# Kernel optimization log

Hardware: AMD Instinct MI355X
Metric: run time of the kernel (lower is better)

The kernel has to match this reference:

```python
import jax, jax.numpy as jnp
import numpy as np

ALPHA = 0.2  # LeakyReLU negative slope


def setup_inputs() -> dict:
    key = jax.random.key(0)
    k1, k2, k3, k4, k5 = jax.random.split(key, 5)
    N, H, W, T, V, F = 8, 64, 64, 32, 32, 32
    h = jax.random.normal(k1, (N, H, W, T, V), dtype=jnp.float32)
    W_map = jax.random.normal(k2, (T, F), dtype=jnp.float32) * (1.414 / np.sqrt(T))
    b_map = jax.random.normal(k3, (F,), dtype=jnp.float32) * 0.01
    a_attn = jax.random.normal(k4, (2 * F, 1), dtype=jnp.float32) * (1.414 / np.sqrt(2 * F))
    B_adj = jax.random.normal(k5, (V, V), dtype=jnp.float32) * 1e-3 + 1e-6
    return {"h": h, "W_map": W_map, "b_map": b_map, "a_attn": a_attn, "B_adj": B_adj}


def reference(h, W_map, b_map, a_attn, B_adj):
    # h: (N,H,W,T,V) -> (N,V,H,W,T)
    hv = jnp.transpose(h, (0, 4, 1, 2, 3))
    Wh = hv @ W_map + b_map  # (N,V,H,W,F) -- LinearMapping
    N, V, H, W, F = Wh.shape
    # pairwise concat + matmul with a decomposes exactly into two projections
    a1, a2 = a_attn[:F, 0], a_attn[F:, 0]
    e = (jnp.einsum('nihwf,f->nihw', Wh, a1)[:, :, None, :, :]
         + jnp.einsum('njhwf,f->njhw', Wh, a2)[:, None, :, :, :])  # (N,V,V,H,W)
    e = jnp.where(e > 0, e, ALPHA * e)  # LeakyReLU
    attn = jax.nn.softmax(e, axis=-1)  # softmax over the W dim (as in original: dim=-1 of (N,V,V,H,W))
    # normalized adjacency: (B + I), min-max scaled, symmetric degree normalization
    adj = B_adj + jnp.eye(V, dtype=B_adj.dtype)
    adj = (adj - adj.min()) / (adj.max() - adj.min())
    d12 = 1.0 / jnp.sqrt(jnp.sum(adj, axis=1))
    adj_n = d12[:, None] * adj * d12[None, :]  # (V,V)
    # weighted aggregation over source vertices j (the original double for-loop)
    hp = jnp.einsum('nijhw,njhwf->inhwf', attn, Wh)  # (V,N,H,W,F)
    # replicate permute(1,3,4,2,0).view(N,H,W*F,V) @ adj_n
    hp = jnp.transpose(hp, (1, 3, 4, 2, 0)).reshape(N, H, W * F, V)
    hp = (hp @ adj_n).reshape(N, H, W, F, V)
    return jax.nn.elu(hp)
```

## Files before the change

kernel.cpp:

```cpp
#include <hip/hip_runtime.h>
#include <math.h>

typedef __attribute__((ext_vector_type(8))) short bf16x8;
typedef __attribute__((ext_vector_type(16))) float f32x16;
typedef __attribute__((ext_vector_type(4))) float f32x4;
typedef __attribute__((ext_vector_type(8))) unsigned short us8;

static constexpr size_t WS_WA   = 0;
static constexpr size_t WS_C12  = 64;
static constexpr size_t WS_WMF  = 96;
static constexpr size_t WS_ADJF = 608;
static constexpr size_t WS_WAB  = 1120;

__device__ __forceinline__ unsigned short f2bf(float x){
    union { float f; unsigned u; } c; c.f = x;
    unsigned r = c.u + 0x7FFFu + ((c.u >> 16) & 1u);
    return (unsigned short)(r >> 16);
}
__device__ __forceinline__ unsigned pk2(float a, float b){
    return (unsigned)f2bf(a) | ((unsigned)f2bf(b) << 16);
}
__device__ __forceinline__ float bf2f(unsigned short v){
    return __uint_as_float(((unsigned)v) << 16);
}
__device__ __forceinline__ float elu(float x){ return x > 0.f ? x : __expf(x) - 1.0f; }
__device__ __forceinline__ float lrelu(float x){ return fmaxf(x, 0.2f * x); }

__global__ __launch_bounds__(1024) void k0_prep(const float* __restrict__ W_map,
    const float* __restrict__ b_map, const float* __restrict__ a_attn,
    const float* __restrict__ B_adj, float* __restrict__ ws)
{
    __shared__ float lds[1024];
    __shared__ float d12[32];
    __shared__ float waS[64];
    int tid = threadIdx.x;
    int i = tid >> 5, j = tid & 31;
    float a = B_adj[tid] + (i == j ? 1.0f : 0.0f);
    lds[tid] = a; __syncthreads();
    for (int s = 512; s > 0; s >>= 1) { if (tid < s) lds[tid] = fmaxf(lds[tid], lds[tid + s]); __syncthreads(); }
    float mx = lds[0]; __syncthreads();
    lds[tid] = a; __syncthreads();
    for (int s = 512; s > 0; s >>= 1) { if (tid < s) lds[tid] = fminf(lds[tid], lds[tid + s]); __syncthreads(); }
    float mn = lds[0]; __syncthreads();
    lds[tid] = (a - mn) / (mx - mn); __syncthreads();
    if (tid < 32) {
        float s = 0.f;
        for (int jj = 0; jj < 32; ++jj) s += lds[tid * 32 + jj];
        d12[tid] = 1.0f / sqrtf(s);
    }
    if (tid < 32) {
        float w1 = 0.f, w2 = 0.f;
        for (int f = 0; f < 32; ++f) {
            w1 += W_map[tid * 32 + f] * a_attn[f];
            w2 += W_map[tid * 32 + f] * a_attn[32 + f];
        }
        waS[tid] = w1; waS[32 + tid] = w2;
        ws[WS_WA + tid] = w1; ws[WS_WA + 32 + tid] = w2;
    }
    __syncthreads();

    {
        int kap = tid >> 9, rem = tid & 511, l = rem >> 3, e = rem & 7;
        int krow = 16 * kap + 8 * (l >> 5) + e;
        int col  = l & 31;
        ((unsigned short*)(ws + WS_WMF))[tid] = f2bf(W_map[krow * 32 + col]);
        float aij = B_adj[krow * 32 + col] + (krow == col ? 1.0f : 0.0f);
        float adjv = d12[krow] * ((aij - mn) / (mx - mn)) * d12[col];
        ((unsigned short*)(ws + WS_ADJF))[tid] = f2bf(adjv);
        float wab = (col == 0) ? waS[krow] : (col == 1) ? waS[32 + krow] : 0.f;
        ((unsigned short*)(ws + WS_WAB))[tid] = f2bf(wab);
    }
    if (tid == 0) {
        float c1 = 0.f, c2 = 0.f;
        for (int f = 0; f < 32; ++f) { c1 += b_map[f] * a_attn[f]; c2 += b_map[f] * a_attn[32 + f]; }
        ws[WS_C12] = c1; ws[WS_C12 + 1] = c2;
    }
}

#if __has_builtin(__builtin_amdgcn_permlane32_swap)
typedef __attribute__((ext_vector_type(2))) unsigned int u32p;
template<int KAP>
__device__ __forceinline__ bf16x8 xform(const f32x16& d, int hi){
    (void)hi;
    unsigned b0 = pk2(d[8*KAP+0], d[8*KAP+1]);
    unsigned b1 = pk2(d[8*KAP+2], d[8*KAP+3]);
    unsigned b2 = pk2(d[8*KAP+4], d[8*KAP+5]);
    unsigned b3 = pk2(d[8*KAP+6], d[8*KAP+7]);
    u32p s02 = __builtin_amdgcn_permlane32_swap(b0, b2, false, false);
    u32p s13 = __builtin_amdgcn_permlane32_swap(b1, b3, false, false);
    union { unsigned u[4]; bf16x8 v; } t;
    t.u[0] = s02[0]; t.u[1] = s13[0]; t.u[2] = s02[1]; t.u[3] = s13[1];
    return t.v;
}
#else
template<int KAP>
__device__ __forceinline__ bf16x8 xform(const f32x16& d, int hi){
    unsigned b0 = pk2(d[8*KAP+0], d[8*KAP+1]);
    unsigned b1 = pk2(d[8*KAP+2], d[8*KAP+3]);
    unsigned b2 = pk2(d[8*KAP+4], d[8*KAP+5]);
    unsigned b3 = pk2(d[8*KAP+6], d[8*KAP+7]);
    unsigned pb0 = (unsigned)__shfl_xor((int)b0, 32, 64);
    unsigned pb1 = (unsigned)__shfl_xor((int)b1, 32, 64);
    unsigned pb2 = (unsigned)__shfl_xor((int)b2, 32, 64);
    unsigned pb3 = (unsigned)__shfl_xor((int)b3, 32, 64);
    union { unsigned u[4]; bf16x8 v; } t;
    t.u[0] = hi ? pb2 : b0;
    t.u[1] = hi ? pb3 : b1;
    t.u[2] = hi ? b2 : pb0;
    t.u[3] = hi ? b3 : pb1;
    return t.v;
}
#endif

__global__ __launch_bounds__(1024, 4) void kfused(const float* __restrict__ hin,
    const float* __restrict__ b_map, const float* __restrict__ ws, float* __restrict__ out)
{
    __shared__ unsigned short hbf[64 * 1024];
    __shared__ float s1L[64 * 32];
    __shared__ float s2L[64 * 32];
    __shared__ float rdenL[1024];

    const int tid = threadIdx.x;
    const int wv = tid >> 6, l = tid & 63;
    const int c = l & 31, hi = l >> 5;
    const int nh = blockIdx.x;
    const int hh = nh & 63, n = nh >> 6;

    const float c1 = ws[WS_C12], c2 = ws[WS_C12 + 1];
    const float bc = b_map[c];

    bf16x8 B1f[2], B2f[2], WaB[2];
    {
        const unsigned short* wmf = (const unsigned short*)(ws + WS_WMF);
        const unsigned short* adf = (const unsigned short*)(ws + WS_ADJF);
        const unsigned short* wab = (const unsigned short*)(ws + WS_WAB);
        B1f[0] = *(const bf16x8*)(wmf + l * 8);
        B1f[1] = *(const bf16x8*)(wmf + 512 + l * 8);
        B2f[0] = *(const bf16x8*)(adf + l * 8);
        B2f[1] = *(const bf16x8*)(adf + 512 + l * 8);
        WaB[0] = *(const bf16x8*)(wab + l * 8);
        WaB[1] = *(const bf16x8*)(wab + 512 + l * 8);
    }

    {
        const float* hrow = hin + (long)nh * 65536;
        const int v = tid & 31;
#pragma unroll
        for (int it = 0; it < 8; ++it) {
            const int gid = it * 32 + (tid >> 5);
            const int site = gid >> 2, kap = (gid >> 1) & 1, hw = gid & 1;
            const float* hp = hrow + site * 1024 + (16 * kap + 8 * hw) * 32 + v;
            float x[8];
#pragma unroll
            for (int e = 0; e < 8; ++e) x[e] = hp[e * 32];
            union { unsigned u[4]; us8 v8; } pk;
            pk.u[0] = pk2(x[0], x[1]); pk.u[1] = pk2(x[2], x[3]);
            pk.u[2] = pk2(x[4], x[5]); pk.u[3] = pk2(x[6], x[7]);
            *(us8*)(hbf + site * 1024 + kap * 512 + (v + 32 * hw) * 8) = pk.v8;
        }
    }
    __syncthreads();

    {
#pragma unroll
        for (int k = 0; k < 4; ++k) {
            const int s = wv * 4 + k;
            const unsigned short* fp = hbf + s * 1024;
            bf16x8 a10 = *(const bf16x8*)(fp + l * 8);
            bf16x8 a11 = *(const bf16x8*)(fp + 512 + l * 8);
            f32x16 ds;
#pragma unroll
            for (int r = 0; r < 16; ++r) ds[r] = 0.f;
            ds = __builtin_amdgcn_mfma_f32_32x32x16_bf16(a10, WaB[0], ds, 0, 0, 0);
            ds = __builtin_amdgcn_mfma_f32_32x32x16_bf16(a11, WaB[1], ds, 0, 0, 0);
            if (c < 2) {
                const float cc = (c == 0) ? c1 : c2;
                float* dst = (c == 0) ? s1L : s2L;
#pragma unroll
                for (int r = 0; r < 16; ++r) {
                    int row = (r & 3) + 8 * (r >> 2) + 4 * hi;
                    dst[s * 32 + row] = ds[r] + cc;
                }
            }
        }
    }
    __syncthreads();

    {
        int i = tid >> 5, j = tid & 31;
        float sum = 0.f;
#pragma unroll
        for (int w = 0; w < 64; ++w)
            sum += __expf(lrelu(s1L[w * 32 + i] + s2L[w * 32 + j]));
        rdenL[tid] = 1.0f / sum;
    }
    __syncthreads();

    const int hh5 = hh >> 5, f3 = hh & 31;
#pragma unroll 2
    for (int k = 0; k < 4; ++k) {
        const int s = wv * 4 + k;
        const unsigned short* fp = hbf + s * 1024;
        bf16x8 a10 = *(const bf16x8*)(fp + l * 8);
        bf16x8 a11 = *(const bf16x8*)(fp + 512 + l * 8);

        f32x16 d1;
#pragma unroll
        for (int r = 0; r < 16; ++r) d1[r] = bc;
        d1 = __builtin_amdgcn_mfma_f32_32x32x16_bf16(a10, B1f[0], d1, 0, 0, 0);
        d1 = __builtin_amdgcn_mfma_f32_32x32x16_bf16(a11, B1f[1], d1, 0, 0, 0);
        bf16x8 A3_0 = xform<0>(d1, hi);
        bf16x8 A3_1 = xform<1>(d1, hi);

        const float s2c = s2L[s * 32 + c];
        f32x4 sa  = *(const f32x4*)&s1L[s * 32 + 8 * hi];
        f32x4 sb  = *(const f32x4*)&s1L[s * 32 + 8 * hi + 4];
        f32x4 sc_ = *(const f32x4*)&s1L[s * 32 + 16 + 8 * hi];
        f32x4 sd  = *(const f32x4*)&s1L[s * 32 + 16 + 8 * hi + 4];
        float q[16];
#pragma unroll
        for (int e = 0; e < 4; ++e) {
            int i0 = 8 * hi + e, i1 = 8 * hi + 4 + e, i2i = 16 + 8 * hi + e, i3 = 16 + 8 * hi + 4 + e;
            q[e]      = __expf(lrelu(sa[e] + s2c))  * rdenL[i0 * 32 + c];
            q[4 + e]  = __expf(lrelu(sb[e] + s2c))  * rdenL[i1 * 32 + c];
            q[8 + e]  = __expf(lrelu(sc_[e] + s2c)) * rdenL[i2i * 32 + c];
            q[12 + e] = __expf(lrelu(sd[e] + s2c))  * rdenL[i3 * 32 + c];
        }
        union { unsigned u[4]; bf16x8 v; } A2_0, A2_1;
        A2_0.u[0] = pk2(q[0], q[1]);   A2_0.u[1] = pk2(q[2], q[3]);
        A2_0.u[2] = pk2(q[4], q[5]);   A2_0.u[3] = pk2(q[6], q[7]);
        A2_1.u[0] = pk2(q[8], q[9]);   A2_1.u[1] = pk2(q[10], q[11]);
        A2_1.u[2] = pk2(q[12], q[13]); A2_1.u[3] = pk2(q[14], q[15]);

        f32x16 d2;
#pragma unroll
        for (int r = 0; r < 16; ++r) d2[r] = 0.f;
        d2 = __builtin_amdgcn_mfma_f32_32x32x16_bf16(A2_0.v, B2f[0], d2, 0, 0, 0);
        d2 = __builtin_amdgcn_mfma_f32_32x32x16_bf16(A2_1.v, B2f[1], d2, 0, 0, 0);
        bf16x8 B3_0 = xform<0>(d2, hi);
        bf16x8 B3_1 = xform<1>(d2, hi);

        f32x16 d3;
#pragma unroll
        for (int r = 0; r < 16; ++r) d3[r] = 0.f;
        d3 = __builtin_amdgcn_mfma_f32_32x32x16_bf16(A3_0, B3_0, d3, 0, 0, 0);
        d3 = __builtin_amdgcn_mfma_f32_32x32x16_bf16(A3_1, B3_1, d3, 0, 0, 0);

        float* ob = out + (((long)(n * 64 + s) * 64) * 32 + f3) * 32 + c;
#pragma unroll
        for (int r = 0; r < 16; ++r) {
            int f = (r & 3) + 8 * (r >> 2) + 4 * hi;
            __builtin_nontemporal_store(elu(d3[r]), ob + (f * 2 + hh5) * 1024);
        }
    }
}

extern "C" void kernel_launch(void* const* d_in, const int* in_sizes, int n_in,
                              void* d_out, int out_size, void* d_ws, size_t ws_size,
                              hipStream_t stream) {
    (void)in_sizes; (void)n_in; (void)out_size; (void)ws_size;
    const float* hin    = (const float*)d_in[0];
    const float* W_map  = (const float*)d_in[1];
    const float* b_map  = (const float*)d_in[2];
    const float* a_attn = (const float*)d_in[3];
    const float* B_adj  = (const float*)d_in[4];
    float* out = (float*)d_out;
    float* ws  = (float*)d_ws;

    hipLaunchKernelGGL(k0_prep, dim3(1),   dim3(1024), 0, stream, W_map, b_map, a_attn, B_adj, ws);
    hipLaunchKernelGGL(kfused,  dim3(512), dim3(1024), 0, stream, hin, b_map, ws, out);
}
```

Before: 65.81 us.

## Drop LDS staging of bf16 input; gather MFMA fragments directly from global

Removes the 128KB shared-memory buffer holding the bf16-converted input and its staging barrier. Each wave now loads and converts its MFMA A-fragments straight from global memory in both passes, so the input is read twice but LDS use drops sharply, which could allow more blocks per CU. The second global read pass may hit in cache or may add memory traffic; both loops are also set to unroll 1.

After: 84.47 us. 1.28x slower.

```diff
diff --git a/kernel.cpp b/kernel.cpp
--- a/kernel.cpp
+++ b/kernel.cpp
@@ -4,7 +4,6 @@
 typedef __attribute__((ext_vector_type(8))) short bf16x8;
 typedef __attribute__((ext_vector_type(16))) float f32x16;
 typedef __attribute__((ext_vector_type(4))) float f32x4;
-typedef __attribute__((ext_vector_type(8))) unsigned short us8;
 
 static constexpr size_t WS_WA   = 0;
 static constexpr size_t WS_C12  = 64;
@@ -19,9 +18,6 @@
 }
 __device__ __forceinline__ unsigned pk2(float a, float b){
     return (unsigned)f2bf(a) | ((unsigned)f2bf(b) << 16);
-}
-__device__ __forceinline__ float bf2f(unsigned short v){
-    return __uint_as_float(((unsigned)v) << 16);
 }
 __device__ __forceinline__ float elu(float x){ return x > 0.f ? x : __expf(x) - 1.0f; }
 __device__ __forceinline__ float lrelu(float x){ return fmaxf(x, 0.2f * x); }
@@ -112,10 +108,25 @@
 }
 #endif
 
+__device__ __forceinline__ void gather_frag(const float* __restrict__ hsite, int l,
+                                            bf16x8& a0, bf16x8& a1){
+    const int v = l & 31, hw = l >> 5;
+    const float* p0 = hsite + (8 * hw) * 32 + v;
+    const float* p1 = hsite + (16 + 8 * hw) * 32 + v;
+    float x[8], y[8];
+#pragma unroll
+    for (int e = 0; e < 8; ++e) { x[e] = p0[e * 32]; y[e] = p1[e * 32]; }
+    union { unsigned u[4]; bf16x8 v8; } ua, ub;
+    ua.u[0] = pk2(x[0], x[1]); ua.u[1] = pk2(x[2], x[3]);
+    ua.u[2] = pk2(x[4], x[5]); ua.u[3] = pk2(x[6], x[7]);
+    ub.u[0] = pk2(y[0], y[1]); ub.u[1] = pk2(y[2], y[3]);
+    ub.u[2] = pk2(y[4], y[5]); ub.u[3] = pk2(y[6], y[7]);
+    a0 = ua.v8; a1 = ub.v8;
+}
+
 __global__ __launch_bounds__(1024, 4) void kfused(const float* __restrict__ hin,
     const float* __restrict__ b_map, const float* __restrict__ ws, float* __restrict__ out)
 {
-    __shared__ unsigned short hbf[64 * 1024];
     __shared__ float s1L[64 * 32];
     __shared__ float s2L[64 * 32];
     __shared__ float rdenL[1024];
@@ -128,6 +139,7 @@
 
     const float c1 = ws[WS_C12], c2 = ws[WS_C12 + 1];
     const float bc = b_map[c];
+    const float* hrow = hin + (long)nh * 65536;
 
     bf16x8 B1f[2], B2f[2], WaB[2];
     {
@@ -142,45 +154,23 @@
         WaB[1] = *(const bf16x8*)(wab + 512 + l * 8);
     }
 
-    {
-        const float* hrow = hin + (long)nh * 65536;
-        const int v = tid & 31;
-#pragma unroll
-        for (int it = 0; it < 8; ++it) {
-            const int gid = it * 32 + (tid >> 5);
-            const int site = gid >> 2, kap = (gid >> 1) & 1, hw = gid & 1;
-            const float* hp = hrow + site * 1024 + (16 * kap + 8 * hw) * 32 + v;
-            float x[8];
-#pragma unroll
-            for (int e = 0; e < 8; ++e) x[e] = hp[e * 32];
-            union { unsigned u[4]; us8 v8; } pk;
-            pk.u[0] = pk2(x[0], x[1]); pk.u[1] = pk2(x[2], x[3]);
-            pk.u[2] = pk2(x[4], x[5]); pk.u[3] = pk2(x[6], x[7]);
-            *(us8*)(hbf + site * 1024 + kap * 512 + (v + 32 * hw) * 8) = pk.v8;
-        }
-    }
-    __syncthreads();
-
-    {
-#pragma unroll
-        for (int k = 0; k < 4; ++k) {
-            const int s = wv * 4 + k;
-            const unsigned short* fp = hbf + s * 1024;
-            bf16x8 a10 = *(const bf16x8*)(fp + l * 8);
-            bf16x8 a11 = *(const bf16x8*)(fp + 512 + l * 8);
-            f32x16 ds;
-#pragma unroll
-            for (int r = 0; r < 16; ++r) ds[r] = 0.f;
-            ds = __builtin_amdgcn_mfma_f32_32x32x16_bf16(a10, WaB[0], ds, 0, 0, 0);
-            ds = __builtin_amdgcn_mfma_f32_32x32x16_bf16(a11, WaB[1], ds, 0, 0, 0);
-            if (c < 2) {
-                const float cc = (c == 0) ? c1 : c2;
-                float* dst = (c == 0) ? s1L : s2L;
-#pragma unroll
-                for (int r = 0; r < 16; ++r) {
-                    int row = (r & 3) + 8 * (r >> 2) + 4 * hi;
-                    dst[s * 32 + row] = ds[r] + cc;
-                }
+#pragma unroll 1
+    for (int k = 0; k < 4; ++k) {
+        const int s = wv * 4 + k;
+        bf16x8 a10, a11;
+        gather_frag(hrow + s * 1024, l, a10, a11);
+        f32x16 ds;
+#pragma unroll
+        for (int r = 0; r < 16; ++r) ds[r] = 0.f;
+        ds = __builtin_amdgcn_mfma_f32_32x32x16_bf16(a10, WaB[0], ds, 0, 0, 0);
+        ds = __builtin_amdgcn_mfma_f32_32x32x16_bf16(a11, WaB[1], ds, 0, 0, 0);
+        if (c < 2) {
+            const float cc = (c == 0) ? c1 : c2;
+            float* dst = (c == 0) ? s1L : s2L;
+#pragma unroll
+            for (int r = 0; r < 16; ++r) {
+                int row = (r & 3) + 8 * (r >> 2) + 4 * hi;
+                dst[s * 32 + row] = ds[r] + cc;
             }
         }
     }
@@ -197,12 +187,11 @@
     __syncthreads();
 
     const int hh5 = hh >> 5, f3 = hh & 31;
-#pragma unroll 2
+#pragma unroll 1
     for (int k = 0; k < 4; ++k) {
         const int s = wv * 4 + k;
-        const unsigned short* fp = hbf + s * 1024;
-        bf16x8 a10 = *(const bf16x8*)(fp + l * 8);
-        bf16x8 a11 = *(const bf16x8*)(fp + 512 + l * 8);
+        bf16x8 a10, a11;
+        gather_frag(hrow + s * 1024, l, a10, a11);
 
         f32x16 d1;
 #pragma unroll
```

## Process two rows per block, prefetching second row during first row's compute

Applied to the files above, without the earlier changes.

Each block now handles two (n,h) rows. It prefetches the second row's global loads while computing the first row's outputs, then reuses the same LDS tile. The gather and attention-score MFMA are fused into one pass without a separate LDS round-trip, the s1/s2 scores are stored as bf16 in LDS, and bf16 conversion switches to the HIP intrinsic. The grid halves to 256 blocks on a 256-CU part and launch_bounds drops the min-blocks hint. Risks are lower occupancy, extra register pressure and reduced score precision.

Result: no change. 66.45 us (+1.0%).

```diff
diff --git a/kernel.cpp b/kernel.cpp
--- a/kernel.cpp
+++ b/kernel.cpp
@@ -1,9 +1,9 @@
 #include <hip/hip_runtime.h>
+#include <hip/hip_bf16.h>
 #include <math.h>
 
 typedef __attribute__((ext_vector_type(8))) short bf16x8;
 typedef __attribute__((ext_vector_type(16))) float f32x16;
-typedef __attribute__((ext_vector_type(4))) float f32x4;
 typedef __attribute__((ext_vector_type(8))) unsigned short us8;
 
 static constexpr size_t WS_WA   = 0;
@@ -17,8 +17,12 @@
     unsigned r = c.u + 0x7FFFu + ((c.u >> 16) & 1u);
     return (unsigned short)(r >> 16);
 }
+__device__ __forceinline__ unsigned short f2bfn(float x){
+    __hip_bfloat16 h = __float2bfloat16(x);
+    union { __hip_bfloat16 h; unsigned short u; } cv; cv.h = h; return cv.u;
+}
 __device__ __forceinline__ unsigned pk2(float a, float b){
-    return (unsigned)f2bf(a) | ((unsigned)f2bf(b) << 16);
+    return (unsigned)f2bfn(a) | ((unsigned)f2bfn(b) << 16);
 }
 __device__ __forceinline__ float bf2f(unsigned short v){
     return __uint_as_float(((unsigned)v) << 16);
@@ -58,7 +62,6 @@
         ws[WS_WA + tid] = w1; ws[WS_WA + 32 + tid] = w2;
     }
     __syncthreads();
-
     {
         int kap = tid >> 9, rem = tid & 511, l = rem >> 3, e = rem & 7;
         int krow = 16 * kap + 8 * (l >> 5) + e;
@@ -112,22 +115,113 @@
 }
 #endif
 
-__global__ __launch_bounds__(1024, 4) void kfused(const float* __restrict__ hin,
+__device__ __forceinline__ void gather_raw(const float* __restrict__ hsite, int l,
+                                           float* __restrict__ x, float* __restrict__ y){
+    const int v = l & 31, hw = l >> 5;
+    const float* p0 = hsite + (8 * hw) * 32 + v;
+    const float* p1 = hsite + (16 + 8 * hw) * 32 + v;
+#pragma unroll
+    for (int e = 0; e < 8; ++e) { x[e] = p0[e * 32]; y[e] = p1[e * 32]; }
+}
+__device__ __forceinline__ bf16x8 pack8(const float* __restrict__ x){
+    union { unsigned u[4]; bf16x8 v8; } t;
+    t.u[0] = pk2(x[0], x[1]); t.u[1] = pk2(x[2], x[3]);
+    t.u[2] = pk2(x[4], x[5]); t.u[3] = pk2(x[6], x[7]);
+    return t.v8;
+}
+
+__device__ __forceinline__ void s12_mfma(bf16x8 a10, bf16x8 a11, const bf16x8* WaB,
+    unsigned short* s1p, unsigned short* s2p, int s, int c, int hi, float c1, float c2)
+{
+    f32x16 ds;
+#pragma unroll
+    for (int r = 0; r < 16; ++r) ds[r] = 0.f;
+    ds = __builtin_amdgcn_mfma_f32_32x32x16_bf16(a10, WaB[0], ds, 0, 0, 0);
+    ds = __builtin_amdgcn_mfma_f32_32x32x16_bf16(a11, WaB[1], ds, 0, 0, 0);
+    if (c < 2) {
+        const float cc = (c == 0) ? c1 : c2;
+        unsigned short* dst = (c == 0) ? s1p : s2p;
+#pragma unroll
+        for (int r = 0; r < 16; ++r) {
+            int row = (r & 3) + 8 * (r >> 2) + 4 * hi;
+            dst[s * 32 + row] = f2bfn(ds[r] + cc);
+        }
+    }
+}
+
+__device__ __forceinline__ void site_compute(const unsigned short* __restrict__ hbf,
+    const unsigned short* __restrict__ s1p, const unsigned short* __restrict__ s2p,
+    const float* __restrict__ rdenL, float* __restrict__ out,
+    int nh, int s, int l, int c, int hi, const bf16x8* B1f, const bf16x8* B2f, float bc)
+{
+    const bf16x8 a10 = *(const bf16x8*)(hbf + s * 1024 + l * 8);
+    const bf16x8 a11 = *(const bf16x8*)(hbf + s * 1024 + 512 + l * 8);
+
+    f32x16 d1;
+#pragma unroll
+    for (int r = 0; r < 16; ++r) d1[r] = bc;
+    d1 = __builtin_amdgcn_mfma_f32_32x32x16_bf16(a10, B1f[0], d1, 0, 0, 0);
+    d1 = __builtin_amdgcn_mfma_f32_32x32x16_bf16(a11, B1f[1], d1, 0, 0, 0);
+    bf16x8 A3_0 = xform<0>(d1, hi);
+    bf16x8 A3_1 = xform<1>(d1, hi);
+
+    const us8 s1a = *(const us8*)(s1p + s * 32 + 8 * hi);
+    const us8 s1c = *(const us8*)(s1p + s * 32 + 16 + 8 * hi);
+    const float s2c = bf2f(s2p[s * 32 + c]);
+    float q[16];
+#pragma unroll
+    for (int e = 0; e < 4; ++e) {
+        q[e]      = __expf(lrelu(bf2f(s1a[e])     + s2c)) * rdenL[(8 * hi + e) * 32 + c];
+        q[4 + e]  = __expf(lrelu(bf2f(s1a[4 + e]) + s2c)) * rdenL[(8 * hi + 4 + e) * 32 + c];
+        q[8 + e]  = __expf(lrelu(bf2f(s1c[e])     + s2c)) * rdenL[(16 + 8 * hi + e) * 32 + c];
+        q[12 + e] = __expf(lrelu(bf2f(s1c[4 + e]) + s2c)) * rdenL[(16 + 8 * hi + 4 + e) * 32 + c];
+    }
+    union { unsigned u[4]; bf16x8 v; } A2_0, A2_1;
+    A2_0.u[0] = pk2(q[0], q[1]);   A2_0.u[1] = pk2(q[2], q[3]);
+    A2_0.u[2] = pk2(q[4], q[5]);   A2_0.u[3] = pk2(q[6], q[7]);
+    A2_1.u[0] = pk2(q[8], q[9]);   A2_1.u[1] = pk2(q[10], q[11]);
+    A2_1.u[2] = pk2(q[12], q[13]); A2_1.u[3] = pk2(q[14], q[15]);
+
+    f32x16 d2;
+#pragma unroll
+    for (int r = 0; r < 16; ++r) d2[r] = 0.f;
+    d2 = __builtin_amdgcn_mfma_f32_32x32x16_bf16(A2_0.v, B2f[0], d2, 0, 0, 0);
+    d2 = __builtin_amdgcn_mfma_f32_32x32x16_bf16(A2_1.v, B2f[1], d2, 0, 0, 0);
+    bf16x8 B3_0 = xform<0>(d2, hi);
+    bf16x8 B3_1 = xform<1>(d2, hi);
+
+    f32x16 d3;
+#pragma unroll
+    for (int r = 0; r < 16; ++r) d3[r] = 0.f;
+    d3 = __builtin_amdgcn_mfma_f32_32x32x16_bf16(A3_0, B3_0, d3, 0, 0, 0);
+    d3 = __builtin_amdgcn_mfma_f32_32x32x16_bf16(A3_1, B3_1, d3, 0, 0, 0);
+
+    const int hh = nh & 63, n = nh >> 6, hh5 = hh >> 5, f3 = hh & 31;
+    float* ob = out + (((long)(n * 64 + s) * 64) * 32 + f3) * 32 + c;
+#pragma unroll
+    for (int r = 0; r < 16; ++r) {
+        int f = (r & 3) + 8 * (r >> 2) + 4 * hi;
+        __builtin_nontemporal_store(elu(d3[r]), ob + (f * 2 + hh5) * 1024);
+    }
+}
+
+__global__ __launch_bounds__(1024) void kfused(const float* __restrict__ hin,
     const float* __restrict__ b_map, const float* __restrict__ ws, float* __restrict__ out)
 {
     __shared__ unsigned short hbf[64 * 1024];
-    __shared__ float s1L[64 * 32];
-    __shared__ float s2L[64 * 32];
+    __shared__ unsigned short s1b[2][2048];
+    __shared__ unsigned short s2b[2][2048];
     __shared__ float rdenL[1024];
 
     const int tid = threadIdx.x;
     const int wv = tid >> 6, l = tid & 63;
     const int c = l & 31, hi = l >> 5;
-    const int nh = blockIdx.x;
-    const int hh = nh & 63, n = nh >> 6;
+    const int nh0 = blockIdx.x * 2, nh1 = nh0 + 1;
 
     const float c1 = ws[WS_C12], c2 = ws[WS_C12 + 1];
     const float bc = b_map[c];
+    const float* hrow0 = hin + (long)nh0 * 65536;
+    const float* hrow1 = hin + (long)nh1 * 65536;
 
     bf16x8 B1f[2], B2f[2], WaB[2];
     {
@@ -142,47 +236,15 @@
         WaB[1] = *(const bf16x8*)(wab + 512 + l * 8);
     }
 
-    {
-        const float* hrow = hin + (long)nh * 65536;
-        const int v = tid & 31;
-#pragma unroll
-        for (int it = 0; it < 8; ++it) {
-            const int gid = it * 32 + (tid >> 5);
-            const int site = gid >> 2, kap = (gid >> 1) & 1, hw = gid & 1;
-            const float* hp = hrow + site * 1024 + (16 * kap + 8 * hw) * 32 + v;
-            float x[8];
-#pragma unroll
-            for (int e = 0; e < 8; ++e) x[e] = hp[e * 32];
-            union { unsigned u[4]; us8 v8; } pk;
-            pk.u[0] = pk2(x[0], x[1]); pk.u[1] = pk2(x[2], x[3]);
-            pk.u[2] = pk2(x[4], x[5]); pk.u[3] = pk2(x[6], x[7]);
-            *(us8*)(hbf + site * 1024 + kap * 512 + (v + 32 * hw) * 8) = pk.v8;
-        }
-    }
-    __syncthreads();
-
-    {
-#pragma unroll
-        for (int k = 0; k < 4; ++k) {
-            const int s = wv * 4 + k;
-            const unsigned short* fp = hbf + s * 1024;
-            bf16x8 a10 = *(const bf16x8*)(fp + l * 8);
-            bf16x8 a11 = *(const bf16x8*)(fp + 512 + l * 8);
-            f32x16 ds;
-#pragma unroll
-            for (int r = 0; r < 16; ++r) ds[r] = 0.f;
-            ds = __builtin_amdgcn_mfma_f32_32x32x16_bf16(a10, WaB[0], ds, 0, 0, 0);
-            ds = __builtin_amdgcn_mfma_f32_32x32x16_bf16(a11, WaB[1], ds, 0, 0, 0);
-            if (c < 2) {
-                const float cc = (c == 0) ? c1 : c2;
-                float* dst = (c == 0) ? s1L : s2L;
-#pragma unroll
-                for (int r = 0; r < 16; ++r) {
-                    int row = (r & 3) + 8 * (r >> 2) + 4 * hi;
-                    dst[s * 32 + row] = ds[r] + cc;
-                }
-            }
-        }
+#pragma unroll
+    for (int k = 0; k < 4; ++k) {
+        const int s = wv * 4 + k;
+        float x[8], y[8];
+        gather_raw(hrow0 + s * 1024, l, x, y);
+        bf16x8 a10 = pack8(x), a11 = pack8(y);
+        *(bf16x8*)(hbf + s * 1024 + l * 8) = a10;
+        *(bf16x8*)(hbf + s * 1024 + 512 + l * 8) = a11;
+        s12_mfma(a10, a11, WaB, s1b[0], s2b[0], s, c, hi, c1, c2);
     }
     __syncthreads();
 
@@ -191,67 +253,38 @@
         float sum = 0.f;
 #pragma unroll
         for (int w = 0; w < 64; ++w)
-            sum += __expf(lrelu(s1L[w * 32 + i] + s2L[w * 32 + j]));
+            sum += __expf(lrelu(bf2f(s1b[0][w * 32 + i]) + bf2f(s2b[0][w * 32 + j])));
         rdenL[tid] = 1.0f / sum;
     }
     __syncthreads();
 
-    const int hh5 = hh >> 5, f3 = hh & 31;
-#pragma unroll 2
+#pragma unroll
     for (int k = 0; k < 4; ++k) {
         const int s = wv * 4 + k;
-        const unsigned short* fp = hbf + s * 1024;
-        bf16x8 a10 = *(const bf16x8*)(fp + l * 8);
-        bf16x8 a11 = *(const bf16x8*)(fp + 512 + l * 8);
-
-        f32x16 d1;
-#pragma unroll
-        for (int r = 0; r < 16; ++r) d1[r] = bc;
-        d1 = __builtin_amdgcn_mfma_f32_32x32x16_bf16(a10, B1f[0], d1, 0, 0, 0);
-        d1 = __builtin_amdgcn_mfma_f32_32x32x16_bf16(a11, B1f[1], d1, 0, 0, 0);
-        bf16x8 A3_0 = xform<0>(d1, hi);
-        bf16x8 A3_1 = xform<1>(d1, hi);
-
-        const float s2c = s2L[s * 32 + c];
-        f32x4 sa  = *(const f32x4*)&s1L[s * 32 + 8 * hi];
-        f32x4 sb  = *(const f32x4*)&s1L[s * 32 + 8 * hi + 4];
-        f32x4 sc_ = *(const f32x4*)&s1L[s * 32 + 16 + 8 * hi];
-        f32x4 sd  = *(const f32x4*)&s1L[s * 32 + 16 + 8 * hi + 4];
-        float q[16];
-#pragma unroll
-        for (int e = 0; e < 4; ++e) {
-            int i0 = 8 * hi + e, i1 = 8 * hi + 4 + e, i2i = 16 + 8 * hi + e, i3 = 16 + 8 * hi + 4 + e;
-            q[e]      = __expf(lrelu(sa[e] + s2c))  * rdenL[i0 * 32 + c];
-            q[4 + e]  = __expf(lrelu(sb[e] + s2c))  * rdenL[i1 * 32 + c];
-            q[8 + e]  = __expf(lrelu(sc_[e] + s2c)) * rdenL[i2i * 32 + c];
-            q[12 + e] = __expf(lrelu(sd[e] + s2c))  * rdenL[i3 * 32 + c];
-        }
-        union { unsigned u[4]; bf16x8 v; } A2_0, A2_1;
-        A2_0.u[0] = pk2(q[0], q[1]);   A2_0.u[1] = pk2(q[2], q[3]);
-        A2_0.u[2] = pk2(q[4], q[5]);   A2_0.u[3] = pk2(q[6], q[7]);
-        A2_1.u[0] = pk2(q[8], q[9]);   A2_1.u[1] = pk2(q[10], q[11]);
-        A2_1.u[2] = pk2(q[12], q[13]); A2_1.u[3] = pk2(q[14], q[15]);
-
-        f32x16 d2;
-#pragma unroll
-        for (int r = 0; r < 16; ++r) d2[r] = 0.f;
-        d2 = __builtin_amdgcn_mfma_f32_32x32x16_bf16(A2_0.v, B2f[0], d2, 0, 0, 0);
-        d2 = __builtin_amdgcn_mfma_f32_32x32x16_bf16(A2_1.v, B2f[1], d2, 0, 0, 0);
-        bf16x8 B3_0 = xform<0>(d2, hi);
-        bf16x8 B3_1 = xform<1>(d2, hi);
-
-        f32x16 d3;
-#pragma unroll
-        for (int r = 0; r < 16; ++r) d3[r] = 0.f;
-        d3 = __builtin_amdgcn_mfma_f32_32x32x16_bf16(A3_0, B3_0, d3, 0, 0, 0);
-        d3 = __builtin_amdgcn_mfma_f32_32x32x16_bf16(A3_1, B3_1, d3, 0, 0, 0);
-
-        float* ob = out + (((long)(n * 64 + s) * 64) * 32 + f3) * 32 + c;
-#pragma unroll
-        for (int r = 0; r < 16; ++r) {
-            int f = (r & 3) + 8 * (r >> 2) + 4 * hi;
-            __builtin_nontemporal_store(elu(d3[r]), ob + (f * 2 + hh5) * 1024);
-        }
+        float px[8], py[8];
+        gather_raw(hrow1 + s * 1024, l, px, py);
+        site_compute(hbf, s1b[0], s2b[0], rdenL, out, nh0, s, l, c, hi, B1f, B2f, bc);
+        bf16x8 pa10 = pack8(px), pa11 = pack8(py);
+        *(bf16x8*)(hbf + s * 1024 + l * 8) = pa10;
+        *(bf16x8*)(hbf + s * 1024 + 512 + l * 8) = pa11;
+        s12_mfma(pa10, pa11, WaB, s1b[1], s2b[1], s, c, hi, c1, c2);
+    }
+    __syncthreads();
+
+    {
+        int i = tid >> 5, j = tid & 31;
+        float sum = 0.f;
+#pragma unroll
+        for (int w = 0; w < 64; ++w)
+            sum += __expf(lrelu(bf2f(s1b[1][w * 32 + i]) + bf2f(s2b[1][w * 32 + j])));
+        rdenL[tid] = 1.0f / sum;
+    }
+    __syncthreads();
+
+#pragma unroll
+    for (int k = 0; k < 4; ++k) {
+        const int s = wv * 4 + k;
+        site_compute(hbf, s1b[1], s2b[1], rdenL, out, nh1, s, l, c, hi, B1f, B2f, bc);
     }
 }
 
@@ -268,5 +301,5 @@
     float* ws  = (float*)d_ws;
 
     hipLaunchKernelGGL(k0_prep, dim3(1),   dim3(1024), 0, stream, W_map, b_map, a_attn, B_adj, ws);
-    hipLaunchKernelGGL(kfused,  dim3(512), dim3(1024), 0, stream, hin, b_map, ws, out);
-}
+    hipLaunchKernelGGL(kfused,  dim3(256), dim3(1024), 0, stream, hin, b_map, ws, out);
+}
```
